# Performance work log

Hardware: AMD Instinct MI355X
Metric: run time of the kernel (lower is better)

The kernel has to match this reference:

```python
import jax, jax.numpy as jnp
import numpy as np

N = 100000   # nodes per graph (single graph per branch; batch vector = all zeros)
E = 400000   # directed edges per graph
F = 64       # input node features
H = 256      # hidden channels
NA = 8       # num_additional resin features
K = int(np.ceil(0.5 * N))  # SAGPooling ratio=0.5 top-k (static, single graph)


def _bn(x, g, b):
    # BatchNorm with track_running_stats=False -> always batch stats, biased var
    m = x.mean(0)
    v = x.var(0)
    return (x - m) * jax.lax.rsqrt(v + 1e-5) * g + b


def _prelu(x, a):
    return jnp.where(x >= 0, x, a[0] * x)


def _gat(x, src, dst, W, a_src, a_dst, bias):
    # PyG GATConv(heads=1, concat=True, negative_slope=0.2, add_self_loops=True), aggr='max'
    n = x.shape[0]
    h = x @ W  # [N,H]
    loop = jnp.arange(n, dtype=src.dtype)
    s = jnp.concatenate([src, loop])
    d = jnp.concatenate([dst, loop])
    e = jax.nn.leaky_relu((h @ a_src)[s] + (h @ a_dst)[d], 0.2)  # [E+N]
    mx = jax.ops.segment_max(e, d, num_segments=n)
    ex = jnp.exp(e - mx[d])
    sm = jax.ops.segment_sum(ex, d, num_segments=n)
    alpha = ex / (sm[d] + 1e-16)  # softmax over incoming edges per target
    out = jax.ops.segment_max(h[s] * alpha[:, None], d, num_segments=n)  # max aggregation
    out = jnp.where(jnp.isfinite(out), out, 0.0)
    return out + bias


def _sage(x, src, dst, Wl, bl, Wr):
    # PyG SAGEConv(aggr='max'): lin_l(max_j x_j) + lin_r(x_i), lin_r has no bias
    agg = jax.ops.segment_max(x[src], dst, num_segments=x.shape[0])
    agg = jnp.where(jnp.isfinite(agg), agg, 0.0)
    return agg @ Wl + bl + x @ Wr


def _sagpool(x, src, dst, Wrel, brel, Wroot):
    # SAGPooling(GraphConv(H,1,aggr='add'), ratio=0.5, nonlinearity=tanh, multiplier=1)
    agg = jax.ops.segment_sum(x[src], dst, num_segments=x.shape[0])
    score = (agg @ Wrel + brel + x @ Wroot)[:, 0]  # [N]
    vals, idx = jax.lax.top_k(score, K)
    return x[idx] * jnp.tanh(vals)[:, None]  # [K,H]


def _branch(x, ei, gat_W, gat_asrc, gat_adst, gat_b, bn1_g, bn1_b, prelu1,
            sage_Wl, sage_bl, sage_Wr, bn2_g, bn2_b, prelu2,
            pool_Wrel, pool_brel, pool_Wroot):
    src, dst = ei[0], ei[1]
    h = _prelu(_bn(_gat(x, src, dst, gat_W, gat_asrc, gat_adst, gat_b), bn1_g, bn1_b), prelu1)
    h = _prelu(_bn(_sage(h, src, dst, sage_Wl, sage_bl, sage_Wr), bn2_g, bn2_b), prelu2)
    return _sagpool(h, src, dst, pool_Wrel, pool_brel, pool_Wroot)


def setup_inputs() -> dict:
    key = jax.random.key(0)
    ks = jax.random.split(key, 8)
    inp = {
        "A_x": jax.random.normal(ks[0], (N, F), jnp.float32),
        "G_x": jax.random.normal(ks[1], (N, F), jnp.float32),
        "add_features": jax.random.normal(ks[2], (NA,), jnp.float32),
        "A_edge_index": jax.random.randint(ks[3], (2, E), 0, N, dtype=jnp.int32),
        "G_edge_index": jax.random.randint(ks[4], (2, E), 0, N, dtype=jnp.int32),
    }

    def bp(k):
        kk = jax.random.split(k, 7)
        s = lambda i, sh: jax.random.normal(kk[i], sh, jnp.float32) * 0.05
        return dict(
            gat_W=s(0, (F, H)), gat_asrc=s(1, (H,)), gat_adst=s(2, (H,)), gat_b=jnp.zeros((H,)),
            bn1_g=jnp.ones((H,)), bn1_b=jnp.zeros((H,)), prelu1=jnp.full((1,), 0.25),
            sage_Wl=s(3, (H, H)), sage_bl=jnp.zeros((H,)), sage_Wr=s(4, (H, H)),
            bn2_g=jnp.ones((H,)), bn2_b=jnp.zeros((H,)), prelu2=jnp.full((1,), 0.25),
            pool_Wrel=s(5, (H, 1)), pool_brel=jnp.zeros((1,)), pool_Wroot=s(6, (H, 1)),
        )

    for pre, k in (("A_", ks[5]), ("G_", ks[6])):
        for nme, v in bp(k).items():
            inp[pre + nme] = v
    kh = jax.random.split(ks[7], 2)
    inp["fc1_W"] = jax.random.normal(kh[0], (2 * H + NA, H), jnp.float32) * 0.05
    inp["fc1_b"] = jnp.zeros((H,))
    inp["prelu_h"] = jnp.full((1,), 0.25)
    inp["fc2_W"] = jax.random.normal(kh[1], (H, 1), jnp.float32) * 0.05
    inp["fc2_b"] = jnp.zeros((1,))
    return inp


def reference(A_x, A_edge_index, G_x, G_edge_index, add_features,
              A_gat_W, A_gat_asrc, A_gat_adst, A_gat_b, A_bn1_g, A_bn1_b, A_prelu1,
              A_sage_Wl, A_sage_bl, A_sage_Wr, A_bn2_g, A_bn2_b, A_prelu2,
              A_pool_Wrel, A_pool_brel, A_pool_Wroot,
              G_gat_W, G_gat_asrc, G_gat_adst, G_gat_b, G_bn1_g, G_bn1_b, G_prelu1,
              G_sage_Wl, G_sage_bl, G_sage_Wr, G_bn2_g, G_bn2_b, G_prelu2,
              G_pool_Wrel, G_pool_brel, G_pool_Wroot,
              fc1_W, fc1_b, prelu_h, fc2_W, fc2_b):
    Ap = (A_gat_W, A_gat_asrc, A_gat_adst, A_gat_b, A_bn1_g, A_bn1_b, A_prelu1,
          A_sage_Wl, A_sage_bl, A_sage_Wr, A_bn2_g, A_bn2_b, A_prelu2,
          A_pool_Wrel, A_pool_brel, A_pool_Wroot)
    Gp = (G_gat_W, G_gat_asrc, G_gat_adst, G_gat_b, G_bn1_g, G_bn1_b, G_prelu1,
          G_sage_Wl, G_sage_bl, G_sage_Wr, G_bn2_g, G_bn2_b, G_prelu2,
          G_pool_Wrel, G_pool_brel, G_pool_Wroot)
    Ae = jnp.max(_branch(A_x, A_edge_index, *Ap), axis=0)
    Ge = jnp.max(_branch(G_x, G_edge_index, *Gp), axis=0)
    z = jnp.concatenate([Ae, Ge, add_features])
    h1 = _prelu(z @ fc1_W + fc1_b, prelu_h)
    return jnp.exp(h1 @ fc2_W + fc2_b)
```

## Files before the change

### kernel.cpp

```cpp
#include <hip/hip_runtime.h>
#include <math.h>

#define NN 100000
#define NE 400000
#define FI 64
#define HH 256
#define KT 50000
#define RPN (NN+1)

typedef unsigned short u16;
typedef __attribute__((ext_vector_type(8))) short bf16x8;
typedef __attribute__((ext_vector_type(4))) short bf16x4;
typedef __attribute__((ext_vector_type(4))) float f32x4;

__device__ __forceinline__ float leaky02(float x){ return x >= 0.f ? x : 0.2f*x; }
__device__ __forceinline__ float preluf(float x, float a){ return x >= 0.f ? x : a*x; }

__device__ __forceinline__ float wredmax(float v){
  #pragma unroll
  for (int o=32;o>0;o>>=1) v = fmaxf(v, __shfl_xor(v, o, 64));
  return v;
}
__device__ __forceinline__ float wredsum(float v){
  #pragma unroll
  for (int o=32;o>0;o>>=1) v += __shfl_xor(v, o, 64);
  return v;
}
__device__ __forceinline__ float qredsum(float v){
  #pragma unroll
  for (int o=8;o>0;o>>=1) v += __shfl_xor(v, o, 64);
  return v;
}

__device__ __forceinline__ void softBarrier(){
  asm volatile("s_waitcnt lgkmcnt(0)" ::: "memory");
  __builtin_amdgcn_s_barrier();
}

__device__ __forceinline__ void atomicMaxF(float* a, float v){
  if (v >= 0.f) atomicMax((int*)a, __float_as_int(v));
  else atomicMin((unsigned int*)a, __float_as_uint(v));
}

__device__ __forceinline__ float4 bnprelu4(float4 v, float4 sc, float4 sh, float a){
  float4 r;
  r.x = preluf(v.x*sc.x+sh.x, a);
  r.y = preluf(v.y*sc.y+sh.y, a);
  r.z = preluf(v.z*sc.z+sh.z, a);
  r.w = preluf(v.w*sc.w+sh.w, a);
  return r;
}

__device__ __forceinline__ u16 f2bf(float f){
  unsigned u = __float_as_uint(f);
  unsigned r = u + 0x7FFFu + ((u>>16)&1u);
  return (u16)(r>>16);
}
__device__ __forceinline__ float bf2f(u16 h){
  return __uint_as_float(((unsigned)h)<<16);
}
__device__ __forceinline__ void split8(float4 a, float4 b, bf16x8& h, bf16x8& l){
  float va[8] = {a.x,a.y,a.z,a.w,b.x,b.y,b.z,b.w};
  #pragma unroll
  for (int j=0;j<8;j++){
    u16 hh = f2bf(va[j]);
    h[j] = (short)hh;
    l[j] = (short)f2bf(va[j] - bf2f(hh));
  }
}
__device__ __forceinline__ void split4(float4 a, bf16x4& h, bf16x4& l){
  float va[4] = {a.x,a.y,a.z,a.w};
  #pragma unroll
  for (int j=0;j<4;j++){
    u16 hh = f2bf(va[j]);
    h[j] = (short)hh;
    l[j] = (short)f2bf(va[j] - bf2f(hh));
  }
}

__global__ void k_count(const int* __restrict__ eiA, const int* __restrict__ eiB, int* __restrict__ deg_){
  int br = blockIdx.y;
  const int* dst = (br ? eiB : eiA) + NE;
  int* deg = deg_ + (size_t)br*NN;
  int e = blockIdx.x*blockDim.x + threadIdx.x;
  if (e < NE) atomicAdd(&deg[dst[e]], 1);
}

__global__ __launch_bounds__(1024) void k_scan1(const int* __restrict__ deg_, int* __restrict__ rowptr_, int* __restrict__ bsums_){
  int br = blockIdx.y;
  const int* deg = deg_ + (size_t)br*NN;
  int* rowptr = rowptr_ + (size_t)br*RPN;
  int* bsums = bsums_ + (size_t)br*128;
  __shared__ int sm[1024];
  int t = threadIdx.x; int g = blockIdx.x*1024 + t;
  int v = (g < NN) ? deg[g] : 0;
  sm[t] = v; __syncthreads();
  for (int o=1;o<1024;o<<=1){
    int add = (t>=o)? sm[t-o] : 0;
    __syncthreads();
    sm[t] += add;
    __syncthreads();
  }
  if (g < NN) rowptr[g] = sm[t] - v;
  if (t == 1023) bsums[blockIdx.x] = sm[1023];
}

__global__ __launch_bounds__(128) void k_scan2(int* __restrict__ bsums_, int nblk){
  int br = blockIdx.y;
  int* bsums = bsums_ + (size_t)br*128;
  __shared__ int sm[128];
  int t = threadIdx.x;
  int v = (t < nblk) ? bsums[t] : 0;
  sm[t] = v; __syncthreads();
  for (int o=1;o<128;o<<=1){
    int add = (t>=o)? sm[t-o] : 0;
    __syncthreads();
    sm[t] += add;
    __syncthreads();
  }
  if (t < nblk) bsums[t] = sm[t] - v;
}

__global__ __launch_bounds__(1024) void k_scan3(int* __restrict__ rowptr_, const int* __restrict__ bsums_, int* __restrict__ cursor_){
  int br = blockIdx.y;
  int* rowptr = rowptr_ + (size_t)br*RPN;
  const int* bsums = bsums_ + (size_t)br*128;
  int* cursor = cursor_ + (size_t)br*NN;
  int g = blockIdx.x*1024 + threadIdx.x;
  if (g < NN){ int r = rowptr[g] + bsums[blockIdx.x]; rowptr[g] = r; cursor[g] = r; }
  if (blockIdx.x==0 && threadIdx.x==0) rowptr[NN] = NE;
}

__global__ void k_scatter(const int* __restrict__ eiA, const int* __restrict__ eiB, int* __restrict__ cursor_, int* __restrict__ adj_){
  int br = blockIdx.y;
  const int* ei = br ? eiB : eiA;
  const int* src = ei;
  const int* dst = ei + NE;
  int* cursor = cursor_ + (size_t)br*NN;
  int* adj = adj_ + (size_t)br*NE;
  int e = blockIdx.x*blockDim.x + threadIdx.x;
  if (e < NE){ int d = dst[e]; int slot = atomicAdd(&cursor[d], 1); adj[slot] = src[e]; }
}

__global__ __launch_bounds__(256) void k_splitW(const float* __restrict__ WrA, const float* __restrict__ WrB,
    const float* __restrict__ WlA, const float* __restrict__ WlB, u16* __restrict__ WtT_){
  int br = blockIdx.y;
  const float* Wr = br ? WrB : WrA;
  const float* Wl = br ? WlB : WlA;
  u16* WtT = WtT_ + (size_t)br*16*16384;
  int idx = blockIdx.x*256 + threadIdx.x;
  int k = idx >> 8, n = idx & 255;
  float v = (k < HH) ? Wr[(size_t)k*HH + n] : Wl[(size_t)(k-HH)*HH + n];
  u16 hi = f2bf(v);
  float lo = v - bf2f(hi);
  size_t base = ((size_t)(k>>5))*16384 + (size_t)((k>>3)&3)*4096 + (size_t)n*8 + (k&7);
  WtT[base] = hi;
  WtT[base + 2048] = f2bf(lo);
}
__global__ __launch_bounds__(256) void k_splitW1(const float* __restrict__ WA, const float* __restrict__ WB, u16* __restrict__ WtT_){
  int br = blockIdx.y;
  const float* W = br ? WB : WA;
  u16* WtT = WtT_ + (size_t)br*2*16384;
  int idx = blockIdx.x*256 + threadIdx.x;
  int k = idx >> 8, n = idx & 255;
  float v = W[(size_t)k*HH + n];
  u16 hi = f2bf(v);
  float lo = v - bf2f(hi);
  size_t base = ((size_t)(k>>5))*16384 + (size_t)((k>>3)&3)*4096 + (size_t)n*8 + (k&7);
  WtT[base] = hi;
  WtT[base + 2048] = f2bf(lo);
}

#define ASTRIDE 528

__global__ __launch_bounds__(256, 2) void k_gemm1(const float* __restrict__ xA, const float* __restrict__ xB,
    const u16* __restrict__ WtT_,
    const float* __restrict__ asA, const float* __restrict__ asB,
    const float* __restrict__ adA, const float* __restrict__ adB,
    float* __restrict__ out_, float* __restrict__ asrc_, float* __restrict__ adst_){
  int br = blockIdx.y;
  const float* x = br ? xB : xA;
  const u16* WtT = WtT_ + (size_t)br*2*16384;
  const float* a_src = br ? asB : asA;
  const float* a_dst = br ? adB : adA;
  float* out = out_ + (size_t)br*NN*HH;
  float* asrc = asrc_ + (size_t)br*NN;
  float* adst = adst_ + (size_t)br*NN;

  __shared__ u16 As[2][8*ASTRIDE];
  int tid = threadIdx.x;
  int row0 = blockIdx.x*64;
  int wave = tid>>6, lane = tid&63;
  int l15 = lane&15, quad = lane>>4;
  int col0 = wave*64;
  int sm_ = tid >> 2, sg = tid & 3;
  int sgrow = row0 + sm_; if (sgrow >= NN) sgrow = NN-1;
  f32x4 acc[4][4];
  #pragma unroll
  for (int mt=0;mt<4;mt++)
    #pragma unroll
    for (int nt=0;nt<4;nt++){ f32x4 z = {0.f,0.f,0.f,0.f}; acc[mt][nt] = z; }

  const u16* bbase = WtT + ((size_t)quad<<12) + (size_t)(col0 + l15)*8;
  bf16x8 B0h[4],B0l[4],B1h[4],B1l[4];
  float4 va0, va1;

  auto loadA = [&](int kc){
    va0 = *((const float4*)(x + (size_t)sgrow*FI + kc + sg*8));
    va1 = *((const float4*)(x + (size_t)sgrow*FI + kc + sg*8 + 4));
  };
  auto writeA = [&](int wb){
    bf16x8 h, l;
    split8(va0, va1, h, l);
    *((bf16x8*)&As[wb][sg*ASTRIDE + sm_*8]) = h;
    *((bf16x8*)&As[wb][(4+sg)*ASTRIDE + sm_*8]) = l;
  };
  auto loadB = [&](int ck, bf16x8 (&Bh)[4], bf16x8 (&Bl)[4]){
    const u16* bb = bbase + ((size_t)ck<<14);
    #pragma unroll
    for (int nt=0;nt<4;nt++){
      Bh[nt] = *((const bf16x8*)(bb + nt*128));
      Bl[nt] = *((const bf16x8*)(bb + 2048 + nt*128));
    }
  };
  auto mmacc = [&](int rb, bf16x8 (&Bh)[4], bf16x8 (&Bl)[4]){
    bf16x8 ah[4], al[4];
    #pragma unroll
    for (int mt=0;mt<4;mt++){
      int m = mt*16 + l15;
      ah[mt] = *((bf16x8*)&As[rb][quad*ASTRIDE + m*8]);
      al[mt] = *((bf16x8*)&As[rb][(4+quad)*ASTRIDE + m*8]);
    }
    #pragma unroll
    for (int nt=0;nt<4;nt++)
      #pragma unroll
      for (int mt=0;mt<4;mt++){
        acc[mt][nt] = __builtin_amdgcn_mfma_f32_16x16x32_bf16(ah[mt], Bh[nt], acc[mt][nt], 0, 0, 0);
        acc[mt][nt] = __builtin_amdgcn_mfma_f32_16x16x32_bf16(al[mt], Bh[nt], acc[mt][nt], 0, 0, 0);
        acc[mt][nt] = __builtin_amdgcn_mfma_f32_16x16x32_bf16(ah[mt], Bl[nt], acc[mt][nt], 0, 0, 0);
      }
  };

  loadA(0);
  writeA(0);
  loadA(32);
  loadB(0, B0h, B0l);
  softBarrier();
  writeA(1);
  loadB(1, B1h, B1l);
  mmacc(0, B0h, B0l);
  softBarrier();
  mmacc(1, B1h, B1l);

  float ps[4][4], pd[4][4];
  #pragma unroll
  for (int mt=0;mt<4;mt++)
    #pragma unroll
    for (int r=0;r<4;r++){ ps[mt][r]=0.f; pd[mt][r]=0.f; }
  #pragma unroll
  for (int nt=0;nt<4;nt++){
    int c = col0 + nt*16 + l15;
    float av = a_src[c], dv = a_dst[c];
    #pragma unroll
    for (int mt=0;mt<4;mt++){
      int gbase = row0 + mt*16 + quad*4;
      #pragma unroll
      for (int r=0;r<4;r++){
        int grow = gbase + r;
        float v = acc[mt][nt][r];
        if (grow < NN) out[(size_t)grow*HH + c] = v;
        ps[mt][r] += v*av; pd[mt][r] += v*dv;
      }
    }
  }
  __syncthreads();
  float* sda = (float*)As;
  float* sdd = sda + 256;
  #pragma unroll
  for (int mt=0;mt<4;mt++)
    #pragma unroll
    for (int r=0;r<4;r++){
      float s = qredsum(ps[mt][r]);
      float d = qredsum(pd[mt][r]);
      if (l15 == 0){
        int row = mt*16 + quad*4 + r;
        sda[wave*64 + row] = s;
        sdd[wave*64 + row] = d;
      }
    }
  __syncthreads();
  if (tid < 64){
    int grow = row0 + tid;
    if (grow < NN){
      asrc[grow] = sda[tid] + sda[64+tid] + sda[128+tid] + sda[192+tid];
      adst[grow] = sdd[tid] + sdd[64+tid] + sdd[128+tid] + sdd[192+tid];
    }
  }
}

__global__ __launch_bounds__(256) void k_gat(const float* __restrict__ h_, const float* __restrict__ asrc_,
     const float* __restrict__ adst_, const int* __restrict__ rowptr_, const int* __restrict__ adj_,
     const float* __restrict__ biasA, const float* __restrict__ biasB, float* __restrict__ out_){
  int br = blockIdx.y;
  const float* h = h_ + (size_t)br*NN*HH;
  const float* asrc = asrc_ + (size_t)br*NN;
  const float* adst = adst_ + (size_t)br*NN;
  const int* rowptr = rowptr_ + (size_t)br*RPN;
  const int* adj = adj_ + (size_t)br*NE;
  const float* bias = br ? biasB : biasA;
  float* out = out_ + (size_t)br*NN*HH;

  int node = blockIdx.x*4 + (threadIdx.x>>6);
  int lane = threadIdx.x & 63;
  int rs = rowptr[node], re = rowptr[node+1];
  int deg = re - rs;
  float adsti = adst[node];
  float eself = leaky02(asrc[node] + adsti);
  int c0 = lane*4;
  float4 acc;
  float4 bv = *((const float4*)&bias[c0]);
  if (deg <= 64){
    bool act = lane < deg;
    int sv = 0; float asv = 0.f;
    if (act){ sv = adj[rs + lane]; asv = asrc[sv]; }
    float e_l = act ? leaky02(asv + adsti) : -INFINITY;
    float m = fmaxf(eself, wredmax(e_l));
    float ex = act ? expf(e_l - m) : 0.f;
    float es = expf(eself - m);
    float denom = wredsum(ex) + es + 1e-16f;
    float aself = es/denom;
    float av = ex/denom;
    float4 hv = *((const float4*)&h[(size_t)node*HH + c0]);
    acc = make_float4(hv.x*aself, hv.y*aself, hv.z*aself, hv.w*aself);
    for (int jj=0; jj<deg; jj++){
      int sb = __shfl(sv, jj, 64);
      float ab = __shfl(av, jj, 64);
      float4 q = *((const float4*)&h[(size_t)sb*HH + c0]);
      acc.x = fmaxf(acc.x, q.x*ab); acc.y = fmaxf(acc.y, q.y*ab);
      acc.z = fmaxf(acc.z, q.z*ab); acc.w = fmaxf(acc.w, q.w*ab);
    }
  } else {
    float m = eself;
    for (int j = rs + lane; j < re; j += 64) m = fmaxf(m, leaky02(asrc[adj[j]] + adsti));
    m = wredmax(m);
    float ssum = 0.f;
    for (int j = rs + lane; j < re; j += 64) ssum += expf(leaky02(asrc[adj[j]] + adsti) - m);
    ssum = wredsum(ssum) + expf(eself - m);
    float denom = ssum + 1e-16f;
    float aself = expf(eself - m)/denom;
    float4 hv = *((const float4*)&h[(size_t)node*HH + c0]);
    acc = make_float4(hv.x*aself, hv.y*aself, hv.z*aself, hv.w*aself);
    for (int jb = rs; jb < re; jb += 64){
      int cnt = min(64, re - jb);
      int sv = 0; float av = 0.f;
      if (lane < cnt){ sv = adj[jb+lane]; av = expf(leaky02(asrc[sv] + adsti) - m)/denom; }
      for (int jj=0; jj<cnt; jj++){
        int sb = __shfl(sv, jj, 64);
        float ab = __shfl(av, jj, 64);
        float4 q = *((const float4*)&h[(size_t)sb*HH + c0]);
        acc.x = fmaxf(acc.x, q.x*ab); acc.y = fmaxf(acc.y, q.y*ab);
        acc.z = fmaxf(acc.z, q.z*ab); acc.w = fmaxf(acc.w, q.w*ab);
      }
    }
  }
  acc.x += bv.x; acc.y += bv.y; acc.z += bv.z; acc.w += bv.w;
  *((float4*)&out[(size_t)node*HH + c0]) = acc;
}

__global__ __launch_bounds__(256) void k_bnstats(const float* __restrict__ x_, float* __restrict__ sums_){
  int br = blockIdx.y;
  const float* x = x_ + (size_t)br*NN*HH;
  float* s_ = sums_ + (size_t)br*2*HH;
  float* q_ = s_ + HH;
  int c = threadIdx.x;
  float s = 0.f, q = 0.f;
  for (int r = blockIdx.x; r < NN; r += gridDim.x){
    float v = x[(size_t)r*HH + c];
    s += v; q += v*v;
  }
  atomicAdd(&s_[c], s);
  atomicAdd(&q_[c], q);
}

__global__ __launch_bounds__(256) void k_bnfin(const float* __restrict__ sums_,
    const float* __restrict__ gA, const float* __restrict__ gB,
    const float* __restrict__ bA, const float* __restrict__ bB,
    float* __restrict__ scale_, float* __restrict__ shift_){
  int br = blockIdx.y;
  const float* sums = sums_ + (size_t)br*2*HH;
  const float* sumsq = sums + HH;
  const float* g = br ? gB : gA;
  const float* b = br ? bB : bA;
  float* scale = scale_ + (size_t)br*HH;
  float* shift = shift_ + (size_t)br*HH;
  int c = threadIdx.x;
  float mean = sums[c]/(float)NN;
  float var = sumsq[c]/(float)NN - mean*mean;
  float rstd = rsqrtf(var + 1e-5f);
  float sc = g[c]*rstd;
  scale[c] = sc; shift[c] = b[c] - mean*sc;
}

__global__ __launch_bounds__(256) void k_sageagg(const float* __restrict__ xin_, const float* __restrict__ scale_,
    const float* __restrict__ shift_, const float* __restrict__ pA, const float* __restrict__ pB,
    const int* __restrict__ rowptr_, const int* __restrict__ adj_, float* __restrict__ agg_){
  int br = blockIdx.y;
  const float* xin = xin_ + (size_t)br*NN*HH;
  const float* scale = scale_ + (size_t)br*HH;
  const float* shift = shift_ + (size_t)br*HH;
  const float* prelu = br ? pB : pA;
  const int* rowptr = rowptr_ + (size_t)br*RPN;
  const int* adj = adj_ + (size_t)br*NE;
  float* agg = agg_ + (size_t)br*NN*HH;

  int node = blockIdx.x*4 + (threadIdx.x>>6);
  int lane = threadIdx.x & 63;
  int rs = rowptr[node], re = rowptr[node+1];
  int c0 = lane*4;
  float slope = prelu[0];
  float4 sc = *((const float4*)&scale[c0]);
  float4 sh = *((const float4*)&shift[c0]);
  float4 acc = make_float4(-INFINITY,-INFINITY,-INFINITY,-INFINITY);
  for (int jb = rs; jb < re; jb += 64){
    int cnt = min(64, re - jb);
    int sv = (lane < cnt) ? adj[jb+lane] : 0;
    for (int jj=0; jj<cnt; jj++){
      int sb = __shfl(sv, jj, 64);
      float4 q = *((const float4*)&xin[(size_t)sb*HH + c0]);
      q = bnprelu4(q, sc, sh, slope);
      acc.x = fmaxf(acc.x, q.x); acc.y = fmaxf(acc.y, q.y);
      acc.z = fmaxf(acc.z, q.z); acc.w = fmaxf(acc.w, q.w);
    }
  }
  if (re == rs) acc = make_float4(0.f,0.f,0.f,0.f);
  *((float4*)&agg[(size_t)node*HH + c0]) = acc;
}

__global__ __launch_bounds__(512, 4) void k_gemm2(const float* __restrict__ graw_, const float* __restrict__ agg_,
    const u16* __restrict__ WtT_,
    const float* __restrict__ scale1_, const float* __restrict__ shift1_,
    const float* __restrict__ p1A, const float* __restrict__ p1B,
    const float* __restrict__ blA, const float* __restrict__ blB,
    float* __restrict__ out_, float* __restrict__ sums_){
  int br = blockIdx.y;
  const float* graw = graw_ + (size_t)br*NN*HH;
  const float* agg = agg_ + (size_t)br*NN*HH;
  const u16* WtT = WtT_ + (size_t)br*16*16384;
  const float* scale1 = scale1_ + (size_t)br*HH;
  const float* shift1 = shift1_ + (size_t)br*HH;
  const float* prelu1 = br ? p1B : p1A;
  const float* bl = br ? blB : blA;
  float* out = out_ + (size_t)br*NN*HH;
  float* sums = sums_ + (size_t)br*2*HH;
  float* sumsq = sums + HH;

  __shared__ u16 As[2][8*ASTRIDE];
  int tid = threadIdx.x;
  int row0 = blockIdx.x*64;
  int wave = tid>>6, lane = tid&63;
  int l15 = lane&15, quad = lane>>4;
  int col0 = wave*32;
  int sm_ = tid >> 3, sg = tid & 7;
  int sgrow = row0 + sm_; if (sgrow >= NN) sgrow = NN-1;
  float slope = prelu1[0];
  f32x4 acc[4][2];
  #pragma unroll
  for (int mt=0;mt<4;mt++)
    #pragma unroll
    for (int nt=0;nt<2;nt++){ f32x4 z = {0.f,0.f,0.f,0.f}; acc[mt][nt] = z; }

  const u16* bbase = WtT + ((size_t)quad<<12) + (size_t)(col0 + l15)*8;
  bf16x8 B0h[2],B0l[2],B1h[2],B1l[2];
  float4 vaA, vaB;

  auto loadA = [&](int kc, float4& dst){
    const float* ab = (kc < HH) ? graw : agg;
    int ac = (kc < HH) ? kc : kc - HH;
    dst = *((const float4*)(ab + (size_t)sgrow*HH + ac + sg*4));
  };
  auto writeA = [&](int kc, int wb, float4 v){
    if (kc < HH){
      int kcol = kc + sg*4;
      v = bnprelu4(v, *((const float4*)(scale1+kcol)), *((const float4*)(shift1+kcol)), slope);
    }
    bf16x4 h, l;
    split4(v, h, l);
    int cell = (sg>>1)*ASTRIDE + sm_*8 + (sg&1)*4;
    *((bf16x4*)&As[wb][cell]) = h;
    *((bf16x4*)&As[wb][cell + 4*ASTRIDE]) = l;
  };
  auto loadB = [&](int ck, bf16x8 (&Bh)[2], bf16x8 (&Bl)[2]){
    const u16* bb = bbase + ((size_t)ck<<14);
    #pragma unroll
    for (int nt=0;nt<2;nt++){
      Bh[nt] = *((const bf16x8*)(bb + nt*128));
      Bl[nt] = *((const bf16x8*)(bb + 2048 + nt*128));
    }
  };
  auto body = [&](int k, int rb, float4& vaW, float4& vaL, bf16x8 (&Bh)[2], bf16x8 (&Bl)[2], bf16x8 (&nBh)[2], bf16x8 (&nBl)[2]){
    softBarrier();
    if (k < 15) writeA((k+1)*32, rb^1, vaW);
    if (k < 13) loadA((k+3)*32, vaW);
    if (k < 15) loadB(k+1, nBh, nBl);
    (void)vaL;
    #pragma unroll
    for (int mt=0;mt<4;mt++){
      int m = mt*16 + l15;
      bf16x8 ah = *((bf16x8*)&As[rb][quad*ASTRIDE + m*8]);
      bf16x8 al = *((bf16x8*)&As[rb][(4+quad)*ASTRIDE + m*8]);
      #pragma unroll
      for (int nt=0;nt<2;nt++){
        acc[mt][nt] = __builtin_amdgcn_mfma_f32_16x16x32_bf16(ah, Bh[nt], acc[mt][nt], 0, 0, 0);
        acc[mt][nt] = __builtin_amdgcn_mfma_f32_16x16x32_bf16(al, Bh[nt], acc[mt][nt], 0, 0, 0);
        acc[mt][nt] = __builtin_amdgcn_mfma_f32_16x16x32_bf16(ah, Bl[nt], acc[mt][nt], 0, 0, 0);
      }
    }
  };

  loadA(0, vaA);
  writeA(0, 0, vaA);
  loadA(32, vaA);
  loadA(64, vaB);
  loadB(0, B0h, B0l);
  #pragma unroll 1
  for (int k=0; k<16; k+=2){
    body(k,   0, vaA, vaB, B0h,B0l, B1h,B1l);
    body(k+1, 1, vaB, vaA, B1h,B1l, B0h,B0l);
  }

  float psum[2], psq[2];
  #pragma unroll
  for (int nt=0;nt<2;nt++){
    int c = col0 + nt*16 + l15;
    float bcol = bl[c];
    float s=0.f, q=0.f;
    #pragma unroll
    for (int mt=0;mt<4;mt++){
      int gbase = row0 + mt*16 + quad*4;
      #pragma unroll
      for (int r=0;r<4;r++){
        int grow = gbase + r;
        float v = acc[mt][nt][r] + bcol;
        if (grow < NN){
          out[(size_t)grow*HH + c] = v;
          s += v; q += v*v;
        }
      }
    }
    psum[nt]=s; psq[nt]=q;
  }
  __syncthreads();
  float* sm2 = (float*)As;
  sm2[tid] = 0.f;
  __syncthreads();
  #pragma unroll
  for (int nt=0;nt<2;nt++){
    int c = col0 + nt*16 + l15;
    atomicAdd(&sm2[c], psum[nt]);
    atomicAdd(&sm2[256+c], psq[nt]);
  }
  __syncthreads();
  if (tid < 256){
    atomicAdd(&sums[tid],  sm2[tid]);
    atomicAdd(&sumsq[tid], sm2[256+tid]);
  }
}

__global__ __launch_bounds__(256) void k_gemv2(const float* __restrict__ x2_, const float* __restrict__ scale2_,
    const float* __restrict__ shift2_, const float* __restrict__ p2A, const float* __restrict__ p2B,
    const float* __restrict__ WrelA, const float* __restrict__ WrelB,
    const float* __restrict__ WrootA, const float* __restrict__ WrootB,
    float* __restrict__ y2_, float* __restrict__ y2r_){
  int br = blockIdx.y;
  const float* x2raw = x2_ + (size_t)br*NN*HH;
  const float* scale2 = scale2_ + (size_t)br*HH;
  const float* shift2 = shift2_ + (size_t)br*HH;
  const float* prelu2 = br ? p2B : p2A;
  const float* Wrel = br ? WrelB : WrelA;
  const float* Wroot = br ? WrootB : WrootA;
  float* y2 = y2_ + (size_t)br*NN;
  float* y2r = y2r_ + (size_t)br*NN;

  int node = blockIdx.x*4 + (threadIdx.x>>6);
  int lane = threadIdx.x & 63;
  int c0 = lane*4;
  float slope = prelu2[0];
  float4 v = *((const float4*)&x2raw[(size_t)node*HH + c0]);
  float4 sc = *((const float4*)&scale2[c0]);
  float4 sh = *((const float4*)&shift2[c0]);
  v = bnprelu4(v, sc, sh, slope);
  float4 wr = *((const float4*)&Wrel[c0]);
  float4 wo = *((const float4*)&Wroot[c0]);
  float pr = v.x*wr.x + v.y*wr.y + v.z*wr.z + v.w*wr.w;
  float po = v.x*wo.x + v.y*wo.y + v.z*wo.z + v.w*wo.w;
  pr = wredsum(pr); po = wredsum(po);
  if (lane==0){ y2[node] = pr; y2r[node] = po; }
}

__global__ void k_score(const int* __restrict__ rowptr_, const int* __restrict__ adj_, const float* __restrict__ y2_,
    const float* __restrict__ y2r_, const float* __restrict__ brelA, const float* __restrict__ brelB,
    float* __restrict__ score_, unsigned* __restrict__ keys_){
  int br = blockIdx.y;
  const int* rowptr = rowptr_ + (size_t)br*RPN;
  const int* adj = adj_ + (size_t)br*NE;
  const float* y2 = y2_ + (size_t)br*NN;
  const float* y2r = y2r_ + (size_t)br*NN;
  const float* brel = br ? brelB : brelA;
  float* score = score_ + (size_t)br*NN;
  unsigned* keys = keys_ + (size_t)br*NN;

  int i = blockIdx.x*blockDim.x + threadIdx.x;
  if (i >= NN) return;
  float s = 0.f;
  int rs = rowptr[i], re = rowptr[i+1];
  for (int j=rs;j<re;j++) s += y2[adj[j]];
  float sc = s + brel[0] + y2r[i];
  score[i] = sc;
  unsigned u = __float_as_uint(sc);
  u = (u & 0x80000000u) ? ~u : (u | 0x80000000u);
  keys[i] = u;
}

__global__ void k_hist1(const unsigned* __restrict__ keys_, unsigned* __restrict__ hist_){
  int br = blockIdx.y;
  const unsigned* keys = keys_ + (size_t)br*NN;
  unsigned* hist = hist_ + (size_t)br*65536;
  int i = blockIdx.x*blockDim.x + threadIdx.x;
  if (i < NN) atomicAdd(&hist[keys[i]>>16], 1u);
}

__global__ __launch_bounds__(256) void k_findbin1(const unsigned* __restrict__ hist_, unsigned* __restrict__ scal_){
  int br = blockIdx.y;
  const unsigned* hist = hist_ + (size_t)br*65536;
  unsigned* scal = scal_ + (size_t)br*16;
  __shared__ unsigned suf[256];
  __shared__ unsigned shc[2];
  int t = threadIdx.x;
  const uint4* h4 = (const uint4*)(hist + t*256);
  unsigned s = 0;
  #pragma unroll 8
  for (int b=0;b<64;b++){ uint4 v = h4[b]; s += v.x+v.y+v.z+v.w; }
  suf[t] = s; __syncthreads();
  #pragma unroll
  for (int o=1;o<256;o<<=1){
    unsigned add = (t+o<256)? suf[t+o] : 0u;
    __syncthreads();
    suf[t] += add;
    __syncthreads();
  }
  unsigned ab = suf[t] - s;
  if (ab < (unsigned)KT && ab + s >= (unsigned)KT){ shc[0] = (unsigned)t; shc[1] = ab; }
  __syncthreads();
  int cb = (int)shc[0]; unsigned runbase = shc[1];
  unsigned f = hist[cb*256 + t];
  suf[t] = f; __syncthreads();
  #pragma unroll
  for (int o=1;o<256;o<<=1){
    unsigned add = (t+o<256)? suf[t+o] : 0u;
    __syncthreads();
    suf[t] += add;
    __syncthreads();
  }
  unsigned ta = runbase + suf[t] - f;
  if (ta < (unsigned)KT && ta + f >= (unsigned)KT){
    scal[0] = (unsigned)(cb*256 + t);
    scal[1] = ta;
  }
}

__global__ void k_hist2(const unsigned* __restrict__ keys_, const unsigned* __restrict__ scal_, unsigned* __restrict__ hist_){
  int br = blockIdx.y;
  const unsigned* keys = keys_ + (size_t)br*NN;
  const unsigned* scal = scal_ + (size_t)br*16;
  unsigned* hist = hist_ + (size_t)br*65536;
  int i = blockIdx.x*blockDim.x + threadIdx.x;
  if (i < NN){ unsigned k = keys[i]; if ((k>>16) == scal[0]) atomicAdd(&hist[k & 0xFFFFu], 1u); }
}

__global__ __launch_bounds__(256) void k_findbin2(const unsigned* __restrict__ hist_, unsigned* __restrict__ scal_){
  int br = blockIdx.y;
  const unsigned* hist = hist_ + (size_t)br*65536;
  unsigned* scal = scal_ + (size_t)br*16;
  __shared__ unsigned suf[256];
  __shared__ unsigned shc[2];
  int t = threadIdx.x;
  unsigned target = (unsigned)KT - scal[1];
  const uint4* h4 = (const uint4*)(hist + t*256);
  unsigned s = 0;
  #pragma unroll 8
  for (int b=0;b<64;b++){ uint4 v = h4[b]; s += v.x+v.y+v.z+v.w; }
  suf[t] = s; __syncthreads();
  #pragma unroll
  for (int o=1;o<256;o<<=1){
    unsigned add = (t+o<256)? suf[t+o] : 0u;
    __syncthreads();
    suf[t] += add;
    __syncthreads();
  }
  unsigned ab = suf[t] - s;
  if (ab < target && ab + s >= target){ shc[0] = (unsigned)t; shc[1] = ab; }
  __syncthreads();
  int cb = (int)shc[0]; unsigned runbase = shc[1];
  unsigned f = hist[cb*256 + t];
  suf[t] = f; __syncthreads();
  #pragma unroll
  for (int o=1;o<256;o<<=1){
    unsigned add = (t+o<256)? suf[t+o] : 0u;
    __syncthreads();
    suf[t] += add;
    __syncthreads();
  }
  unsigned ta = runbase + suf[t] - f;
  if (ta < target && ta + f >= target){
    scal[2] = (scal[0] << 16) | (unsigned)(cb*256 + t);
    scal[3] = target - ta;
    scal[4] = f;
  }
}

__global__ void k_select(const unsigned* __restrict__ keys_, const float* __restrict__ score_,
    unsigned* __restrict__ scal_, int* __restrict__ selidx_, float* __restrict__ tvals_){
  int br = blockIdx.y;
  const unsigned* keys = keys_ + (size_t)br*NN;
  const float* score = score_ + (size_t)br*NN;
  unsigned* scal = scal_ + (size_t)br*16;
  int* selidx = selidx_ + (size_t)br*NN;
  float* tvals = tvals_ + (size_t)br*NN;

  int i = blockIdx.x*blockDim.x + threadIdx.x;
  if (i >= NN) return;
  unsigned T = scal[2], needed = scal[3], cnteq = scal[4];
  unsigned k = keys[i];
  int s = 0;
  if (k > T) s = 1;
  else if (k == T){
    if (cnteq <= needed) s = 1;
    else {
      unsigned rank = 0;
      for (int j=0;j<i;j++) rank += (keys[j] == T) ? 1u : 0u;
      s = (rank < needed) ? 1 : 0;
    }
  }
  if (s){
    unsigned idx = atomicAdd(&scal[8], 1u);
    selidx[idx] = i;
    tvals[idx] = tanhf(score[i]);
  }
}

__global__ __launch_bounds__(256) void k_embed(const float* __restrict__ x2_, const float* __restrict__ scale2_,
    const float* __restrict__ shift2_, const float* __restrict__ p2A, const float* __restrict__ p2B,
    const int* __restrict__ selidx_, const float* __restrict__ tvals_, float* __restrict__ embed){
  int br = blockIdx.y;
  const float* x2raw = x2_ + (size_t)br*NN*HH;
  const float* scale2 = scale2_ + (size_t)br*HH;
  const float* shift2 = shift2_ + (size_t)br*HH;
  const float* prelu2 = br ? p2B : p2A;
  const int* selidx = selidx_ + (size_t)br*NN;
  const float* tvals = tvals_ + (size_t)br*NN;

  int c = threadIdx.x;
  float slope = prelu2[0];
  float scv = scale2[c], shv = shift2[c];
  float best = -INFINITY;
  for (int j = blockIdx.x; j < KT; j += gridDim.x){
    int r = selidx[j];
    float v = x2raw[(size_t)r*HH + c]*scv + shv;
    v = preluf(v, slope);
    best = fmaxf(best, v*tvals[j]);
  }
  atomicMaxF(&embed[(size_t)br*HH + c], best);
}

__global__ void k_initembed(float* __restrict__ embed){
  int i = threadIdx.x;
  if (i < 2*HH) embed[i] = -INFINITY;
}

__global__ __launch_bounds__(256) void k_head(const float* __restrict__ embed, const float* __restrict__ addf,
    const float* __restrict__ fc1W, const float* __restrict__ fc1b, const float* __restrict__ preluh,
    const float* __restrict__ fc2W, const float* __restrict__ fc2b, float* __restrict__ out){
  __shared__ float z[2*HH + 8];
  __shared__ float h1s[HH];
  __shared__ float red[4];
  int t = threadIdx.x;
  for (int i=t;i<2*HH;i+=256) z[i] = embed[i];
  if (t < 8) z[2*HH + t] = addf[t];
  __syncthreads();
  float acc = fc1b[t];
  for (int k=0;k<2*HH+8;k++) acc += z[k]*fc1W[(size_t)k*HH + t];
  float slope = preluh[0];
  h1s[t] = preluf(acc, slope);
  __syncthreads();
  float p = h1s[t]*fc2W[t];
  p = wredsum(p);
  if ((t & 63) == 0) red[t>>6] = p;
  __syncthreads();
  if (t == 0) out[0] = expf(red[0]+red[1]+red[2]+red[3] + fc2b[0]);
}

extern "C" void kernel_launch(void* const* d_in, const int* in_sizes, int n_in,
                              void* d_out, int out_size, void* d_ws, size_t ws_size,
                              hipStream_t stream) {
  (void)in_sizes; (void)n_in; (void)out_size;
  char* ws = (char*)d_ws;

  float *bufA, *bufB, *asrc, *adst, *sums, *scale1, *shift1, *scale2, *shift2;
  float *y2, *y2r, *score, *tvals, *embed;
  int *rowptr, *adj, *cursor, *bsums, *selidx;
  unsigned *keys, *hist1, *hist2, *scal;
  u16 *WtT, *WtT1;

  auto doAlloc = [&](int nb)->size_t{
    size_t o = 0;
    auto al = [&](size_t bytes)->char*{ char* p = ws + o; o = (o + bytes + 255) & ~(size_t)255; return p; };
    bufA   = (float*)al((size_t)nb*NN*HH*4);
    bufB   = (float*)al((size_t)nb*NN*HH*4);
    asrc   = (float*)al((size_t)nb*NN*4);
    adst   = (float*)al((size_t)nb*NN*4);
    rowptr = (int*)  al((size_t)nb*RPN*4);
    adj    = (int*)  al((size_t)nb*NE*4);
    cursor = (int*)  al((size_t)nb*NN*4);
    bsums  = (int*)  al((size_t)nb*128*4);
    sums   = (float*)al((size_t)nb*2*HH*4);
    scale1 = (float*)al((size_t)nb*HH*4);
    shift1 = (float*)al((size_t)nb*HH*4);
    scale2 = (float*)al((size_t)nb*HH*4);
    shift2 = (float*)al((size_t)nb*HH*4);
    y2     = (float*)al((size_t)nb*NN*4);
    y2r    = (float*)al((size_t)nb*NN*4);
    score  = (float*)al((size_t)nb*NN*4);
    keys   = (unsigned*)al((size_t)nb*NN*4);
    selidx = (int*)  al((size_t)nb*NN*4);
    tvals  = (float*)al((size_t)nb*NN*4);
    hist1  = (unsigned*)al((size_t)nb*65536*4);
    hist2  = (unsigned*)al((size_t)nb*65536*4);
    scal   = (unsigned*)al((size_t)nb*64);
    embed  = (float*)al((size_t)2*HH*4);
    WtT    = (u16*)al((size_t)nb*16*16384*2);
    WtT1   = (u16*)al((size_t)nb*2*16384*2);
    return o;
  };

  int NB = 2;
  if (doAlloc(2) > ws_size) NB = 1;
  doAlloc(NB);

  const float* addf = (const float*)d_in[2];

  k_initembed<<<dim3(1), dim3(512), 0, stream>>>(embed);

  int nIter = (NB==2) ? 1 : 2;
  for (int it = 0; it < nIter; ++it){
    const float *xA, *xB; const int *eiA, *eiB; int pa, pb;
    if (NB == 2){
      xA = (const float*)d_in[0]; xB = (const float*)d_in[1];
      eiA = (const int*)d_in[3]; eiB = (const int*)d_in[4];
      pa = 5; pb = 21;
    } else {
      xA = xB = (const float*)d_in[it];
      eiA = eiB = (const int*)d_in[3+it];
      pa = pb = (it==0) ? 5 : 21;
    }
    auto PA = [&](int i){ return (const float*)d_in[pa+i]; };
    auto PB = [&](int i){ return (const float*)d_in[pb+i]; };

    hipMemsetAsync(cursor, 0, (size_t)NB*NN*4, stream);
    k_count<<<dim3((NE+255)/256, NB), dim3(256), 0, stream>>>(eiA, eiB, cursor);
    k_scan1<<<dim3(98, NB), dim3(1024), 0, stream>>>(cursor, rowptr, bsums);
    k_scan2<<<dim3(1, NB), dim3(128), 0, stream>>>(bsums, 98);
    k_scan3<<<dim3(98, NB), dim3(1024), 0, stream>>>(rowptr, bsums, cursor);
    k_scatter<<<dim3((NE+255)/256, NB), dim3(256), 0, stream>>>(eiA, eiB, cursor, adj);

    k_splitW<<<dim3(512, NB), dim3(256), 0, stream>>>(PA(9), PB(9), PA(7), PB(7), WtT);
    k_splitW1<<<dim3(64, NB), dim3(256), 0, stream>>>(PA(0), PB(0), WtT1);

    k_gemm1<<<dim3((NN+63)/64, NB), dim3(256), 0, stream>>>(xA, xB, WtT1,
        PA(1), PB(1), PA(2), PB(2), bufA, asrc, adst);
    k_gat<<<dim3(25000, NB), dim3(256), 0, stream>>>(bufA, asrc, adst, rowptr, adj, PA(3), PB(3), bufB);

    hipMemsetAsync(sums, 0, (size_t)NB*2*HH*4, stream);
    k_bnstats<<<dim3(512, NB), dim3(256), 0, stream>>>(bufB, sums);
    k_bnfin<<<dim3(1, NB), dim3(256), 0, stream>>>(sums, PA(4), PB(4), PA(5), PB(5), scale1, shift1);

    k_sageagg<<<dim3(25000, NB), dim3(256), 0, stream>>>(bufB, scale1, shift1, PA(6), PB(6), rowptr, adj, bufA);
    hipMemsetAsync(sums, 0, (size_t)NB*2*HH*4, stream);
    k_gemm2<<<dim3((NN+63)/64, NB), dim3(512), 0, stream>>>(bufB, bufA, WtT,
        scale1, shift1, PA(6), PB(6), PA(8), PB(8), bufB, sums);
    k_bnfin<<<dim3(1, NB), dim3(256), 0, stream>>>(sums, PA(10), PB(10), PA(11), PB(11), scale2, shift2);

    k_gemv2<<<dim3(25000, NB), dim3(256), 0, stream>>>(bufB, scale2, shift2, PA(12), PB(12),
        PA(13), PB(13), PA(15), PB(15), y2, y2r);
    k_score<<<dim3((NN+255)/256, NB), dim3(256), 0, stream>>>(rowptr, adj, y2, y2r, PA(14), PB(14), score, keys);
    hipMemsetAsync(scal, 0, (size_t)NB*64, stream);
    hipMemsetAsync(hist1, 0, (size_t)NB*65536*4, stream);
    hipMemsetAsync(hist2, 0, (size_t)NB*65536*4, stream);
    k_hist1<<<dim3((NN+255)/256, NB), dim3(256), 0, stream>>>(keys, hist1);
    k_findbin1<<<dim3(1, NB), dim3(256), 0, stream>>>(hist1, scal);
    k_hist2<<<dim3((NN+255)/256, NB), dim3(256), 0, stream>>>(keys, scal, hist2);
    k_findbin2<<<dim3(1, NB), dim3(256), 0, stream>>>(hist2, scal);
    k_select<<<dim3((NN+255)/256, NB), dim3(256), 0, stream>>>(keys, score, scal, selidx, tvals);
    float* embDst = (NB==2) ? embed : (embed + it*HH);
    k_embed<<<dim3(256, NB), dim3(256), 0, stream>>>(bufB, scale2, shift2, PA(12), PB(12), selidx, tvals, embDst);
  }

  k_head<<<dim3(1), dim3(256), 0, stream>>>(embed, addf,
      (const float*)d_in[37], (const float*)d_in[38], (const float*)d_in[39],
      (const float*)d_in[40], (const float*)d_in[41], (float*)d_out);
}
```

Baseline: 1.496 ms.

## Enlarge gemm2 row tile, merge weight-split kernels, fuse histogram into score

```diff
diff --git a/kernel.cpp b/kernel.cpp
--- a/kernel.cpp
+++ b/kernel.cpp
@@ -63,15 +63,6 @@
   float va[8] = {a.x,a.y,a.z,a.w,b.x,b.y,b.z,b.w};
   #pragma unroll
   for (int j=0;j<8;j++){
-    u16 hh = f2bf(va[j]);
-    h[j] = (short)hh;
-    l[j] = (short)f2bf(va[j] - bf2f(hh));
-  }
-}
-__device__ __forceinline__ void split4(float4 a, bf16x4& h, bf16x4& l){
-  float va[4] = {a.x,a.y,a.z,a.w};
-  #pragma unroll
-  for (int j=0;j<4;j++){
     u16 hh = f2bf(va[j]);
     h[j] = (short)hh;
     l[j] = (short)f2bf(va[j] - bf2f(hh));
@@ -142,36 +133,39 @@
   if (e < NE){ int d = dst[e]; int slot = atomicAdd(&cursor[d], 1); adj[slot] = src[e]; }
 }
 
-__global__ __launch_bounds__(256) void k_splitW(const float* __restrict__ WrA, const float* __restrict__ WrB,
-    const float* __restrict__ WlA, const float* __restrict__ WlB, u16* __restrict__ WtT_){
-  int br = blockIdx.y;
-  const float* Wr = br ? WrB : WrA;
-  const float* Wl = br ? WlB : WlA;
-  u16* WtT = WtT_ + (size_t)br*16*16384;
-  int idx = blockIdx.x*256 + threadIdx.x;
-  int k = idx >> 8, n = idx & 255;
-  float v = (k < HH) ? Wr[(size_t)k*HH + n] : Wl[(size_t)(k-HH)*HH + n];
-  u16 hi = f2bf(v);
-  float lo = v - bf2f(hi);
-  size_t base = ((size_t)(k>>5))*16384 + (size_t)((k>>3)&3)*4096 + (size_t)n*8 + (k&7);
-  WtT[base] = hi;
-  WtT[base + 2048] = f2bf(lo);
-}
-__global__ __launch_bounds__(256) void k_splitW1(const float* __restrict__ WA, const float* __restrict__ WB, u16* __restrict__ WtT_){
-  int br = blockIdx.y;
-  const float* W = br ? WB : WA;
-  u16* WtT = WtT_ + (size_t)br*2*16384;
-  int idx = blockIdx.x*256 + threadIdx.x;
-  int k = idx >> 8, n = idx & 255;
-  float v = W[(size_t)k*HH + n];
-  u16 hi = f2bf(v);
-  float lo = v - bf2f(hi);
-  size_t base = ((size_t)(k>>5))*16384 + (size_t)((k>>3)&3)*4096 + (size_t)n*8 + (k&7);
-  WtT[base] = hi;
-  WtT[base + 2048] = f2bf(lo);
+__global__ __launch_bounds__(256) void k_splitWall(const float* __restrict__ WrA, const float* __restrict__ WrB,
+    const float* __restrict__ WlA, const float* __restrict__ WlB,
+    const float* __restrict__ WgA, const float* __restrict__ WgB,
+    u16* __restrict__ WtT_, u16* __restrict__ WtT1_){
+  int br = blockIdx.y;
+  if (blockIdx.x < 512){
+    const float* Wr = br ? WrB : WrA;
+    const float* Wl = br ? WlB : WlA;
+    u16* WtT = WtT_ + (size_t)br*16*16384;
+    int idx = blockIdx.x*256 + threadIdx.x;
+    int k = idx >> 8, n = idx & 255;
+    float v = (k < HH) ? Wr[(size_t)k*HH + n] : Wl[(size_t)(k-HH)*HH + n];
+    u16 hi = f2bf(v);
+    float lo = v - bf2f(hi);
+    size_t base = ((size_t)(k>>5))*16384 + (size_t)((k>>3)&3)*4096 + (size_t)n*8 + (k&7);
+    WtT[base] = hi;
+    WtT[base + 2048] = f2bf(lo);
+  } else {
+    const float* W = br ? WgB : WgA;
+    u16* WtT = WtT1_ + (size_t)br*2*16384;
+    int idx = (blockIdx.x-512)*256 + threadIdx.x;
+    int k = idx >> 8, n = idx & 255;
+    float v = W[(size_t)k*HH + n];
+    u16 hi = f2bf(v);
+    float lo = v - bf2f(hi);
+    size_t base = ((size_t)(k>>5))*16384 + (size_t)((k>>3)&3)*4096 + (size_t)n*8 + (k&7);
+    WtT[base] = hi;
+    WtT[base + 2048] = f2bf(lo);
+  }
 }
 
 #define ASTRIDE 528
+#define ASTRIDE2 1040
 
 __global__ __launch_bounds__(256, 2) void k_gemm1(const float* __restrict__ xA, const float* __restrict__ xB,
     const u16* __restrict__ WtT_,
@@ -436,7 +430,7 @@
   *((float4*)&agg[(size_t)node*HH + c0]) = acc;
 }
 
-__global__ __launch_bounds__(512, 4) void k_gemm2(const float* __restrict__ graw_, const float* __restrict__ agg_,
+__global__ __launch_bounds__(512, 3) void k_gemm2(const float* __restrict__ graw_, const float* __restrict__ agg_,
     const u16* __restrict__ WtT_,
     const float* __restrict__ scale1_, const float* __restrict__ shift1_,
     const float* __restrict__ p1A, const float* __restrict__ p1B,
@@ -454,40 +448,41 @@
   float* sums = sums_ + (size_t)br*2*HH;
   float* sumsq = sums + HH;
 
-  __shared__ u16 As[2][8*ASTRIDE];
+  __shared__ u16 As[2][8*ASTRIDE2];
   int tid = threadIdx.x;
-  int row0 = blockIdx.x*64;
+  int row0 = blockIdx.x*128;
   int wave = tid>>6, lane = tid&63;
   int l15 = lane&15, quad = lane>>4;
   int col0 = wave*32;
-  int sm_ = tid >> 3, sg = tid & 7;
+  int sm_ = tid >> 2, sg = tid & 3;
   int sgrow = row0 + sm_; if (sgrow >= NN) sgrow = NN-1;
   float slope = prelu1[0];
-  f32x4 acc[4][2];
-  #pragma unroll
-  for (int mt=0;mt<4;mt++)
+  f32x4 acc[8][2];
+  #pragma unroll
+  for (int mt=0;mt<8;mt++)
     #pragma unroll
     for (int nt=0;nt<2;nt++){ f32x4 z = {0.f,0.f,0.f,0.f}; acc[mt][nt] = z; }
 
   const u16* bbase = WtT + ((size_t)quad<<12) + (size_t)(col0 + l15)*8;
   bf16x8 B0h[2],B0l[2],B1h[2],B1l[2];
-  float4 vaA, vaB;
-
-  auto loadA = [&](int kc, float4& dst){
+  float4 vaA0, vaA1, vaB0, vaB1;
+
+  auto loadA = [&](int kc, float4& d0, float4& d1){
     const float* ab = (kc < HH) ? graw : agg;
     int ac = (kc < HH) ? kc : kc - HH;
-    dst = *((const float4*)(ab + (size_t)sgrow*HH + ac + sg*4));
+    d0 = *((const float4*)(ab + (size_t)sgrow*HH + ac + sg*8));
+    d1 = *((const float4*)(ab + (size_t)sgrow*HH + ac + sg*8 + 4));
   };
-  auto writeA = [&](int kc, int wb, float4 v){
+  auto writeA = [&](int kc, int wb, float4 v0, float4 v1){
     if (kc < HH){
-      int kcol = kc + sg*4;
-      v = bnprelu4(v, *((const float4*)(scale1+kcol)), *((const float4*)(shift1+kcol)), slope);
-    }
-    bf16x4 h, l;
-    split4(v, h, l);
-    int cell = (sg>>1)*ASTRIDE + sm_*8 + (sg&1)*4;
-    *((bf16x4*)&As[wb][cell]) = h;
-    *((bf16x4*)&As[wb][cell + 4*ASTRIDE]) = l;
+      int kcol = kc + sg*8;
+      v0 = bnprelu4(v0, *((const float4*)(scale1+kcol)),   *((const float4*)(shift1+kcol)),   slope);
+      v1 = bnprelu4(v1, *((const float4*)(scale1+kcol+4)), *((const float4*)(shift1+kcol+4)), slope);
+    }
+    bf16x8 h, l;
+    split8(v0, v1, h, l);
+    *((bf16x8*)&As[wb][sg*ASTRIDE2 + sm_*8]) = h;
+    *((bf16x8*)&As[wb][(4+sg)*ASTRIDE2 + sm_*8]) = l;
   };
   auto loadB = [&](int ck, bf16x8 (&Bh)[2], bf16x8 (&Bl)[2]){
     const u16* bb = bbase + ((size_t)ck<<14);
@@ -497,17 +492,16 @@
       Bl[nt] = *((const bf16x8*)(bb + 2048 + nt*128));
     }
   };
-  auto body = [&](int k, int rb, float4& vaW, float4& vaL, bf16x8 (&Bh)[2], bf16x8 (&Bl)[2], bf16x8 (&nBh)[2], bf16x8 (&nBl)[2]){
+  auto body = [&](int k, int rb, float4& vW0, float4& vW1, bf16x8 (&Bh)[2], bf16x8 (&Bl)[2], bf16x8 (&nBh)[2], bf16x8 (&nBl)[2]){
     softBarrier();
-    if (k < 15) writeA((k+1)*32, rb^1, vaW);
-    if (k < 13) loadA((k+3)*32, vaW);
+    if (k < 15) writeA((k+1)*32, rb^1, vW0, vW1);
+    if (k < 13) loadA((k+3)*32, vW0, vW1);
     if (k < 15) loadB(k+1, nBh, nBl);
-    (void)vaL;
-    #pragma unroll
-    for (int mt=0;mt<4;mt++){
+    #pragma unroll
+    for (int mt=0;mt<8;mt++){
       int m = mt*16 + l15;
-      bf16x8 ah = *((bf16x8*)&As[rb][quad*ASTRIDE + m*8]);
-      bf16x8 al = *((bf16x8*)&As[rb][(4+quad)*ASTRIDE + m*8]);
+      bf16x8 ah = *((bf16x8*)&As[rb][quad*ASTRIDE2 + m*8]);
+      bf16x8 al = *((bf16x8*)&As[rb][(4+quad)*ASTRIDE2 + m*8]);
       #pragma unroll
       for (int nt=0;nt<2;nt++){
         acc[mt][nt] = __builtin_amdgcn_mfma_f32_16x16x32_bf16(ah, Bh[nt], acc[mt][nt], 0, 0, 0);
@@ -517,15 +511,15 @@
     }
   };
 
-  loadA(0, vaA);
-  writeA(0, 0, vaA);
-  loadA(32, vaA);
-  loadA(64, vaB);
+  loadA(0, vaA0, vaA1);
+  writeA(0, 0, vaA0, vaA1);
+  loadA(32, vaA0, vaA1);
+  loadA(64, vaB0, vaB1);
   loadB(0, B0h, B0l);
   #pragma unroll 1
   for (int k=0; k<16; k+=2){
-    body(k,   0, vaA, vaB, B0h,B0l, B1h,B1l);
-    body(k+1, 1, vaB, vaA, B1h,B1l, B0h,B0l);
+    body(k,   0, vaA0, vaA1, B0h,B0l, B1h,B1l);
+    body(k+1, 1, vaB0, vaB1, B1h,B1l, B0h,B0l);
   }
 
   float psum[2], psq[2];
@@ -535,7 +529,7 @@
     float bcol = bl[c];
     float s=0.f, q=0.f;
     #pragma unroll
-    for (int mt=0;mt<4;mt++){
+    for (int mt=0;mt<8;mt++){
       int gbase = row0 + mt*16 + quad*4;
       #pragma unroll
       for (int r=0;r<4;r++){
@@ -599,7 +593,7 @@
 
 __global__ void k_score(const int* __restrict__ rowptr_, const int* __restrict__ adj_, const float* __restrict__ y2_,
     const float* __restrict__ y2r_, const float* __restrict__ brelA, const float* __restrict__ brelB,
-    float* __restrict__ score_, unsigned* __restrict__ keys_){
+    float* __restrict__ score_, unsigned* __restrict__ keys_, unsigned* __restrict__ hist_){
   int br = blockIdx.y;
   const int* rowptr = rowptr_ + (size_t)br*RPN;
   const int* adj = adj_ + (size_t)br*NE;
@@ -608,6 +602,7 @@
   const float* brel = br ? brelB : brelA;
   float* score = score_ + (size_t)br*NN;
   unsigned* keys = keys_ + (size_t)br*NN;
+  unsigned* hist = hist_ + (size_t)br*65536;
 
   int i = blockIdx.x*blockDim.x + threadIdx.x;
   if (i >= NN) return;
@@ -619,14 +614,7 @@
   unsigned u = __float_as_uint(sc);
   u = (u & 0x80000000u) ? ~u : (u | 0x80000000u);
   keys[i] = u;
-}
-
-__global__ void k_hist1(const unsigned* __restrict__ keys_, unsigned* __restrict__ hist_){
-  int br = blockIdx.y;
-  const unsigned* keys = keys_ + (size_t)br*NN;
-  unsigned* hist = hist_ + (size_t)br*65536;
-  int i = blockIdx.x*blockDim.x + threadIdx.x;
-  if (i < NN) atomicAdd(&hist[keys[i]>>16], 1u);
+  atomicAdd(&hist[u>>16], 1u);
 }
 
 __global__ __launch_bounds__(256) void k_findbin1(const unsigned* __restrict__ hist_, unsigned* __restrict__ scal_){
@@ -872,8 +860,7 @@
     k_scan3<<<dim3(98, NB), dim3(1024), 0, stream>>>(rowptr, bsums, cursor);
     k_scatter<<<dim3((NE+255)/256, NB), dim3(256), 0, stream>>>(eiA, eiB, cursor, adj);
 
-    k_splitW<<<dim3(512, NB), dim3(256), 0, stream>>>(PA(9), PB(9), PA(7), PB(7), WtT);
-    k_splitW1<<<dim3(64, NB), dim3(256), 0, stream>>>(PA(0), PB(0), WtT1);
+    k_splitWall<<<dim3(576, NB), dim3(256), 0, stream>>>(PA(9), PB(9), PA(7), PB(7), PA(0), PB(0), WtT, WtT1);
 
     k_gemm1<<<dim3((NN+63)/64, NB), dim3(256), 0, stream>>>(xA, xB, WtT1,
         PA(1), PB(1), PA(2), PB(2), bufA, asrc, adst);
@@ -885,17 +872,16 @@
 
     k_sageagg<<<dim3(25000, NB), dim3(256), 0, stream>>>(bufB, scale1, shift1, PA(6), PB(6), rowptr, adj, bufA);
     hipMemsetAsync(sums, 0, (size_t)NB*2*HH*4, stream);
-    k_gemm2<<<dim3((NN+63)/64, NB), dim3(512), 0, stream>>>(bufB, bufA, WtT,
+    k_gemm2<<<dim3((NN+127)/128, NB), dim3(512), 0, stream>>>(bufB, bufA, WtT,
         scale1, shift1, PA(6), PB(6), PA(8), PB(8), bufB, sums);
     k_bnfin<<<dim3(1, NB), dim3(256), 0, stream>>>(sums, PA(10), PB(10), PA(11), PB(11), scale2, shift2);
 
-    k_gemv2<<<dim3(25000, NB), dim3(256), 0, stream>>>(bufB, scale2, shift2, PA(12), PB(12),
-        PA(13), PB(13), PA(15), PB(15), y2, y2r);
-    k_score<<<dim3((NN+255)/256, NB), dim3(256), 0, stream>>>(rowptr, adj, y2, y2r, PA(14), PB(14), score, keys);
     hipMemsetAsync(scal, 0, (size_t)NB*64, stream);
     hipMemsetAsync(hist1, 0, (size_t)NB*65536*4, stream);
     hipMemsetAsync(hist2, 0, (size_t)NB*65536*4, stream);
-    k_hist1<<<dim3((NN+255)/256, NB), dim3(256), 0, stream>>>(keys, hist1);
+    k_gemv2<<<dim3(25000, NB), dim3(256), 0, stream>>>(bufB, scale2, shift2, PA(12), PB(12),
+        PA(13), PB(13), PA(15), PB(15), y2, y2r);
+    k_score<<<dim3((NN+255)/256, NB), dim3(256), 0, stream>>>(rowptr, adj, y2, y2r, PA(14), PB(14), score, keys, hist1);
     k_findbin1<<<dim3(1, NB), dim3(256), 0, stream>>>(hist1, scal);
     k_hist2<<<dim3((NN+255)/256, NB), dim3(256), 0, stream>>>(keys, scal, hist2);
     k_findbin2<<<dim3(1, NB), dim3(256), 0, stream>>>(hist2, scal);
```

New measurement: 1.519 ms. Within noise of the previous version (+1.5%).
